# Kernel tuning notes

Measured on AMD Instinct MI355X. Metric: run time of the kernel, lower is better.

The kernel has to match this reference:

```python
import jax, jax.numpy as jnp
import numpy as np

S, M, E = 8192, 4096, 64          # tokens, model_dim, num_experts
CAPACITY_FACTOR = 1.0
MIN_CAPACITY = 8
CAPACITY = max(int(np.ceil(S / E * CAPACITY_FACTOR)), MIN_CAPACITY)  # 128


def setup_inputs() -> dict:
    key = jax.random.key(0)
    k1, k2 = jax.random.split(key)
    x = jax.random.normal(k1, (S, M), dtype=jnp.float32)
    wg = jax.random.normal(k2, (E, M), dtype=jnp.float32) * (1.0 / np.sqrt(M))
    return {"x": x, "wg": wg}


def reference(x, wg):
    # gate projection (Linear, no bias): logits [s, e]
    logits = jnp.einsum('sm,em->se', x, wg)
    gates = jax.nn.softmax(logits, axis=1)                      # [s, e]

    # top-1 expert per token
    indices1_s = jnp.argmax(gates, axis=1)                      # [s]
    mask1 = jax.nn.one_hot(indices1_s, E, dtype=jnp.int32)      # [s, e]
    exp_counts = jnp.sum(mask1, axis=0)                         # [e]

    # load-balancing aux loss
    me = jnp.mean(gates, axis=0)
    ce = jnp.mean(mask1.astype(jnp.float32), axis=0)
    l_aux = jnp.sum(me * ce) * E

    # capacity drop (use_rts=False): keep first CAPACITY tokens per expert.
    # torch: top_idx = topk(mask1, capacity, dim=0)[1]; scatter ones at those rows.
    top_idx = jax.lax.top_k(mask1.T, CAPACITY)[1]               # [e, c] token ids
    keep = jnp.zeros((S, E), dtype=jnp.int32).at[top_idx.T, jnp.arange(E)[None, :]].set(1)
    mask1 = mask1 * keep                                        # [s, e]

    # position of each token inside its expert's buffer
    locations1 = jnp.cumsum(mask1, axis=0) - 1                  # [s, e]
    locations1_s = jnp.sum(locations1 * mask1, axis=1)          # [s]

    mask1_f = mask1.astype(gates.dtype)
    gates_masked = gates * mask1_f                              # [s, e]
    locations1_sc = jax.nn.one_hot(locations1_s, CAPACITY, dtype=jnp.float32)  # [s, c]

    combine_weights = jnp.einsum('se,sc->sec', gates_masked, locations1_sc)    # [s, e, c]
    dispatch_mask = combine_weights.astype(bool)
    return l_aux, combine_weights, dispatch_mask, exp_counts
```

## Files before the change

kernel.cpp:

```cpp
#include <hip/hip_runtime.h>
#include <hip/hip_bf16.h>

#define TS 8192
#define TM 4096
#define TE 64
#define TCAP 128
#define KS 8
#define KCHUNK (TM / KS)
#define BK 16
#define NTILE (KCHUNK / BK)
#define BM 128
#define GEMM_BLOCKS 512
#define K1_GRID 2048
#define NFILL (K1_GRID - GEMM_BLOCKS)

constexpr size_t CWsz = (size_t)TS * TE * TCAP;
constexpr size_t NOUT = 1 + 2 * CWsz + TE;
constexpr size_t NF4  = (NOUT - 1) / 4;

typedef float v4f __attribute__((ext_vector_type(4)));

__global__ __launch_bounds__(256) void k1_fill_gemm(
    const float* __restrict__ x, const float* __restrict__ wg,
    float* __restrict__ part, float* __restrict__ me, float* __restrict__ out) {
  const int tid = threadIdx.x;
  const int v = (blockIdx.x * 5) & (K1_GRID - 1);

  __shared__ float As[BK][132];
  __shared__ float Ws[BK][68];

  if (v >= GEMM_BLOCKS) {
    const int fid = v - GEMM_BLOCKS;
    const v4f z = {0.f, 0.f, 0.f, 0.f};
    v4f* o4 = (v4f*)out;
    for (size_t i = (size_t)fid * 256 + tid; i < NF4; i += (size_t)NFILL * 256)
      __builtin_nontemporal_store(z, &o4[i]);
    if (fid == 0) {
      if (tid == 0) out[NOUT - 1] = 0.0f;
      if (tid < TE) me[tid] = 0.0f;
    }
    return;
  }

  const int gid = v;
  const int t0 = (gid & 63) * BM;
  const int k0 = (gid >> 6) * KCHUNK;
  const int tg = tid >> 3;
  const int eg = tid & 7;

  float acc[4][8] = {};
  float4 ra[2], rw;

  auto load = [&](int kt) {
    const int kb = k0 + kt * BK;
#pragma unroll
    for (int i = 0; i < 2; i++) {
      int idx = tid + 256 * i;
      int tok = idx >> 2, c4 = idx & 3;
      ra[i] = *(const float4*)&x[(size_t)(t0 + tok) * TM + kb + 4 * c4];
    }
    { int e = tid >> 2, c4 = tid & 3;
      rw = *(const float4*)&wg[(size_t)e * TM + kb + 4 * c4]; }
  };

  load(0);
  for (int kt = 0; kt < NTILE; kt++) {
#pragma unroll
    for (int i = 0; i < 2; i++) {
      int idx = tid + 256 * i;
      int tok = idx >> 2, c4 = idx & 3;
      As[4 * c4 + 0][tok] = ra[i].x; As[4 * c4 + 1][tok] = ra[i].y;
      As[4 * c4 + 2][tok] = ra[i].z; As[4 * c4 + 3][tok] = ra[i].w;
    }
    { int e = tid >> 2, c4 = tid & 3;
      Ws[4 * c4 + 0][e] = rw.x; Ws[4 * c4 + 1][e] = rw.y;
      Ws[4 * c4 + 2][e] = rw.z; Ws[4 * c4 + 3][e] = rw.w; }
    __syncthreads();
    if (kt + 1 < NTILE) load(kt + 1);
#pragma unroll
    for (int k = 0; k < BK; k++) {
      float4 a  = *(const float4*)&As[k][tg * 4];
      float4 b0 = *(const float4*)&Ws[k][eg * 8];
      float4 b1 = *(const float4*)&Ws[k][eg * 8 + 4];
      float av[4] = {a.x, a.y, a.z, a.w};
      float bv[8] = {b0.x, b0.y, b0.z, b0.w, b1.x, b1.y, b1.z, b1.w};
#pragma unroll
      for (int i = 0; i < 4; i++)
#pragma unroll
        for (int j = 0; j < 8; j++) acc[i][j] += av[i] * bv[j];
    }
    __syncthreads();
  }
  float* dst = part + (size_t)(gid >> 6) * TS * TE;
#pragma unroll
  for (int i = 0; i < 4; i++) {
    int tok = t0 + tg * 4 + i;
    *(float4*)&dst[(size_t)tok * TE + eg * 8] =
        make_float4(acc[i][0], acc[i][1], acc[i][2], acc[i][3]);
    *(float4*)&dst[(size_t)tok * TE + eg * 8 + 4] =
        make_float4(acc[i][4], acc[i][5], acc[i][6], acc[i][7]);
  }
}

__global__ __launch_bounds__(256) void k2_softmax(
    const float* __restrict__ part, float* __restrict__ gate1,
    int* __restrict__ idx1, float* __restrict__ me) {
  const int tid = threadIdx.x, w = tid >> 6, lane = tid & 63;
  const int s0 = blockIdx.x * 32;
  float mesum = 0.0f;
  for (int it = 0; it < 8; it++) {
    const int s = s0 + it * 4 + w;
    float logit = 0.0f;
#pragma unroll
    for (int p = 0; p < KS; p++)
      logit += part[((size_t)p * TS + s) * TE + lane];
    float mv = logit; int mi = lane;
#pragma unroll
    for (int off = 32; off; off >>= 1) {
      float ov = __shfl_xor(mv, off);
      int oi = __shfl_xor(mi, off);
      if (ov > mv || (ov == mv && oi < mi)) { mv = ov; mi = oi; }
    }
    float ex = expf(logit - mv);
    float sum = ex;
#pragma unroll
    for (int off = 32; off; off >>= 1) sum += __shfl_xor(sum, off);
    float g = ex / sum;
    mesum += g;
    if (lane == mi) { gate1[s] = g; idx1[s] = mi; }
  }
  __shared__ float red[4][64];
  red[w][lane] = mesum;
  __syncthreads();
  if (w == 0)
    atomicAdd(&me[lane], red[0][lane] + red[1][lane] + red[2][lane] + red[3][lane]);
}

__global__ __launch_bounds__(256) void k3_rank_scatter(
    const int* __restrict__ idx1, const float* __restrict__ gate1,
    int* __restrict__ counts, float* __restrict__ out) {
  const int e = blockIdx.x;
  const int w = threadIdx.x >> 6, lane = threadIdx.x & 63;
  const int s0 = w * (TS / 4);
  __shared__ int wcnt[4];

  int cnt = 0;
  for (int c = 0; c < TS / 4 / 64; c++) {
    int s = s0 + c * 64 + lane;
    cnt += __popcll(__ballot(idx1[s] == e));
  }
  if (lane == 0) wcnt[w] = cnt;
  __syncthreads();
  int base = 0;
  for (int j = 0; j < w; j++) base += wcnt[j];

  for (int c = 0; c < TS / 4 / 64; c++) {
    int s = s0 + c * 64 + lane;
    bool m = (idx1[s] == e);
    unsigned long long mask = __ballot(m);
    if (m) {
      int p = base + __popcll(mask & ((1ull << lane) - 1ull));
      if (p < TCAP) {
        size_t off = 1 + ((size_t)s * TE + e) * (size_t)TCAP + (size_t)p;
        out[off] = gate1[s];
        out[off + CWsz] = 1.0f;
      }
    }
    base += __popcll(mask);
  }
  if (w == 3 && lane == 0) counts[e] = base;
}

__global__ void k4_laux(const float* __restrict__ me, const int* __restrict__ cnts,
                        float* __restrict__ out) {
  const int lane = threadIdx.x;
  float vv = (me[lane] / (float)TS) * ((float)cnts[lane] / (float)TS);
  float sum = vv;
#pragma unroll
  for (int off = 32; off; off >>= 1) sum += __shfl_xor(sum, off);
  if (lane == 0) out[0] = sum * (float)TE;
  out[1 + 2 * CWsz + lane] = (float)cnts[lane];
}

extern "C" void kernel_launch(void* const* d_in, const int* in_sizes, int n_in,
                              void* d_out, int out_size, void* d_ws, size_t ws_size,
                              hipStream_t stream) {
  const float* x  = (const float*)d_in[0];
  const float* wg = (const float*)d_in[1];
  float* out = (float*)d_out;

  float* part  = (float*)d_ws;
  float* gate1 = part + (size_t)KS * TS * TE;
  int*   idx1  = (int*)(gate1 + TS);
  float* me    = (float*)(idx1 + TS);
  int*   cnts  = (int*)(me + TE);

  k1_fill_gemm<<<K1_GRID, 256, 0, stream>>>(x, wg, part, me, out);
  k2_softmax<<<TS / 32, 256, 0, stream>>>(part, gate1, idx1, me);
  k3_rank_scatter<<<TE, 256, 0, stream>>>(idx1, gate1, cnts, out);
  k4_laux<<<1, 64, 0, stream>>>(me, cnts, out);
}
```

Baseline: 698.7 us.

## Fuse softmax into GEMM via last-block counters and fold l_aux into scatter

The split-K GEMM blocks now increment a per-tile atomic counter, and the last block to finish each token tile reduces the partial logits and runs the softmax/argmax for those 128 tokens. The separate softmax kernel is removed. The rank-scatter kernel likewise uses a done counter so its last block computes l_aux and writes the expert counts, which removes the one-block fourth kernel. A memset now zeroes the `me` and counter buffers, trading two kernel launches for one memset plus threadfence/atomic overhead and serialized softmax work in a few tail blocks.

```diff
diff --git a/kernel.cpp b/kernel.cpp
--- a/kernel.cpp
+++ b/kernel.cpp
@@ -17,40 +17,38 @@
 constexpr size_t CWsz = (size_t)TS * TE * TCAP;
 constexpr size_t NOUT = 1 + 2 * CWsz + TE;
 constexpr size_t NF4  = (NOUT - 1) / 4;
+constexpr size_t FSTRIDE = (size_t)NFILL * 256;
 
 typedef float v4f __attribute__((ext_vector_type(4)));
 
-__global__ __launch_bounds__(256) void k1_fill_gemm(
+__global__ __launch_bounds__(256) void k1_gemm_fill_softmax(
     const float* __restrict__ x, const float* __restrict__ wg,
-    float* __restrict__ part, float* __restrict__ me, float* __restrict__ out) {
+    float* __restrict__ part, float* __restrict__ gate1, int* __restrict__ idx1,
+    float* __restrict__ me, int* __restrict__ tilecnt, float* __restrict__ out) {
   const int tid = threadIdx.x;
-  const int v = (blockIdx.x * 5) & (K1_GRID - 1);
+  const int v = (int)((blockIdx.x * 5u) & (K1_GRID - 1));
 
   __shared__ float As[BK][132];
   __shared__ float Ws[BK][68];
+  __shared__ int lastf;
 
   if (v >= GEMM_BLOCKS) {
     const int fid = v - GEMM_BLOCKS;
     const v4f z = {0.f, 0.f, 0.f, 0.f};
     v4f* o4 = (v4f*)out;
-    for (size_t i = (size_t)fid * 256 + tid; i < NF4; i += (size_t)NFILL * 256)
+    for (size_t i = (size_t)fid * 256 + tid; i < NF4; i += FSTRIDE)
       __builtin_nontemporal_store(z, &o4[i]);
-    if (fid == 0) {
-      if (tid == 0) out[NOUT - 1] = 0.0f;
-      if (tid < TE) me[tid] = 0.0f;
-    }
     return;
   }
 
-  const int gid = v;
-  const int t0 = (gid & 63) * BM;
-  const int k0 = (gid >> 6) * KCHUNK;
+  const int tile = v & 63;
+  const int t0 = tile * BM;
+  const int k0 = (v >> 6) * KCHUNK;
   const int tg = tid >> 3;
   const int eg = tid & 7;
 
   float acc[4][8] = {};
   float4 ra[2], rw;
-
   auto load = [&](int kt) {
     const int kb = k0 + kt * BK;
 #pragma unroll
@@ -62,7 +60,6 @@
     { int e = tid >> 2, c4 = tid & 3;
       rw = *(const float4*)&wg[(size_t)e * TM + kb + 4 * c4]; }
   };
-
   load(0);
   for (int kt = 0; kt < NTILE; kt++) {
 #pragma unroll
@@ -91,7 +88,7 @@
     }
     __syncthreads();
   }
-  float* dst = part + (size_t)(gid >> 6) * TS * TE;
+  float* dst = part + (size_t)(v >> 6) * TS * TE;
 #pragma unroll
   for (int i = 0; i < 4; i++) {
     int tok = t0 + tg * 4 + i;
@@ -100,16 +97,17 @@
     *(float4*)&dst[(size_t)tok * TE + eg * 8 + 4] =
         make_float4(acc[i][4], acc[i][5], acc[i][6], acc[i][7]);
   }
-}
-
-__global__ __launch_bounds__(256) void k2_softmax(
-    const float* __restrict__ part, float* __restrict__ gate1,
-    int* __restrict__ idx1, float* __restrict__ me) {
-  const int tid = threadIdx.x, w = tid >> 6, lane = tid & 63;
-  const int s0 = blockIdx.x * 32;
+
+  __threadfence();
+  if (tid == 0) lastf = (atomicAdd(&tilecnt[tile], 1) == KS - 1) ? 1 : 0;
+  __syncthreads();
+  if (!lastf) return;
+  __threadfence();
+
+  const int w = tid >> 6, lane = tid & 63;
   float mesum = 0.0f;
-  for (int it = 0; it < 8; it++) {
-    const int s = s0 + it * 4 + w;
+  for (int it = 0; it < 32; it++) {
+    const int s = t0 + w * 32 + it;
     float logit = 0.0f;
 #pragma unroll
     for (int p = 0; p < KS; p++)
@@ -129,26 +127,26 @@
     mesum += g;
     if (lane == mi) { gate1[s] = g; idx1[s] = mi; }
   }
-  __shared__ float red[4][64];
-  red[w][lane] = mesum;
+  float* lds = &As[0][0];
+  lds[w * 64 + lane] = mesum;
   __syncthreads();
   if (w == 0)
-    atomicAdd(&me[lane], red[0][lane] + red[1][lane] + red[2][lane] + red[3][lane]);
+    atomicAdd(&me[lane], lds[lane] + lds[64 + lane] + lds[128 + lane] + lds[192 + lane]);
 }
 
-__global__ __launch_bounds__(256) void k3_rank_scatter(
+__global__ __launch_bounds__(256) void k2_rank_scatter_laux(
     const int* __restrict__ idx1, const float* __restrict__ gate1,
-    int* __restrict__ counts, float* __restrict__ out) {
+    const float* __restrict__ me, int* __restrict__ cnts, int* __restrict__ done,
+    float* __restrict__ out) {
   const int e = blockIdx.x;
   const int w = threadIdx.x >> 6, lane = threadIdx.x & 63;
   const int s0 = w * (TS / 4);
   __shared__ int wcnt[4];
+  __shared__ int lastf;
 
   int cnt = 0;
-  for (int c = 0; c < TS / 4 / 64; c++) {
-    int s = s0 + c * 64 + lane;
-    cnt += __popcll(__ballot(idx1[s] == e));
-  }
+  for (int c = 0; c < TS / 4 / 64; c++)
+    cnt += __popcll(__ballot(idx1[s0 + c * 64 + lane] == e));
   if (lane == 0) wcnt[w] = cnt;
   __syncthreads();
   int base = 0;
@@ -168,18 +166,22 @@
     }
     base += __popcll(mask);
   }
-  if (w == 3 && lane == 0) counts[e] = base;
-}
-
-__global__ void k4_laux(const float* __restrict__ me, const int* __restrict__ cnts,
-                        float* __restrict__ out) {
-  const int lane = threadIdx.x;
-  float vv = (me[lane] / (float)TS) * ((float)cnts[lane] / (float)TS);
-  float sum = vv;
-#pragma unroll
-  for (int off = 32; off; off >>= 1) sum += __shfl_xor(sum, off);
-  if (lane == 0) out[0] = sum * (float)TE;
-  out[1 + 2 * CWsz + lane] = (float)cnts[lane];
+  if (w == 3 && lane == 0) {
+    cnts[e] = base;
+    __threadfence();
+    lastf = (atomicAdd(done, 1) == TE - 1) ? 1 : 0;
+  }
+  __syncthreads();
+  if (lastf && w == 0) {
+    __threadfence();
+    int c = cnts[lane];
+    float vv = (me[lane] / (float)TS) * ((float)c / (float)TS);
+    float sum = vv;
+#pragma unroll
+    for (int off = 32; off; off >>= 1) sum += __shfl_xor(sum, off);
+    if (lane == 0) out[0] = sum * (float)TE;
+    out[1 + 2 * CWsz + lane] = (float)c;
+  }
 }
 
 extern "C" void kernel_launch(void* const* d_in, const int* in_sizes, int n_in,
@@ -189,14 +191,17 @@
   const float* wg = (const float*)d_in[1];
   float* out = (float*)d_out;
 
-  float* part  = (float*)d_ws;
-  float* gate1 = part + (size_t)KS * TS * TE;
-  int*   idx1  = (int*)(gate1 + TS);
-  float* me    = (float*)(idx1 + TS);
-  int*   cnts  = (int*)(me + TE);
-
-  k1_fill_gemm<<<K1_GRID, 256, 0, stream>>>(x, wg, part, me, out);
-  k2_softmax<<<TS / 32, 256, 0, stream>>>(part, gate1, idx1, me);
-  k3_rank_scatter<<<TE, 256, 0, stream>>>(idx1, gate1, cnts, out);
-  k4_laux<<<1, 64, 0, stream>>>(me, cnts, out);
+  float* part    = (float*)d_ws;
+  float* gate1   = part + (size_t)KS * TS * TE;
+  int*   idx1    = (int*)(gate1 + TS);
+  float* me      = (float*)(idx1 + TS);
+  int*   tilecnt = (int*)(me + TE);
+  int*   done    = tilecnt + TE;
+  int*   cnts    = done + 1;
+
+  hipMemsetAsync(me, 0, (TE + TE + 1) * sizeof(int), stream);
+
+  k1_gemm_fill_softmax<<<K1_GRID, 256, 0, stream>>>(x, wg, part, gate1, idx1,
+                                                    me, tilecnt, out);
+  k2_rank_scatter_laux<<<TE, 256, 0, stream>>>(idx1, gate1, me, cnts, done, out);
 }
```

New measurement: 808.8 us. +15.8%, slower.
